# Performance work log

Measured on AMD Instinct MI355X. Metric: run time of the kernel, lower is better.

The kernel has to match this reference:

```python
import jax, jax.numpy as jnp
import numpy as np

B, C, H, W = 4, 512, 48, 48
BN_EPS = 1e-5


def setup_inputs() -> dict:
    key = jax.random.key(0)
    ks = jax.random.split(key, 12)
    s = 1.0 / np.sqrt(C)  # conv2d default init scale for 1x1 kernels
    return {
        "x": jax.random.normal(ks[0], (B, C, H, W), dtype=jnp.float32),
        "from_depth_estimation": jax.random.normal(ks[1], (B, C, H, W), dtype=jnp.float32),
        "w_rgb": jax.random.uniform(ks[2], (C, C), jnp.float32, -s, s),
        "b_rgb": jax.random.uniform(ks[3], (C,), jnp.float32, -s, s),
        "w_lhs": jax.random.uniform(ks[4], (C, C), jnp.float32, -s, s),
        "b_lhs": jax.random.uniform(ks[5], (C,), jnp.float32, -s, s),
        "w_rhs": jax.random.uniform(ks[6], (C, C), jnp.float32, -s, s),
        "b_rhs": jax.random.uniform(ks[7], (C,), jnp.float32, -s, s),
        "w_dec": jax.random.uniform(ks[8], (C, C), jnp.float32, -s, s),
        "b_dec": jax.random.uniform(ks[9], (C,), jnp.float32, -s, s),
        "gamma": jnp.ones((C,), jnp.float32),
        "beta": jnp.zeros((C,), jnp.float32),
    }


def _to_tokens(t):
    # (B,C,H,W) -> (B*H*W, C)
    return t.transpose(0, 2, 3, 1).reshape(-1, t.shape[1])


def reference(x, from_depth_estimation, w_rgb, b_rgb, w_lhs, b_lhs, w_rhs, b_rhs,
              w_dec, b_dec, gamma, beta):
    # 1x1 convs == per-token linear layers; weight layout (out, in)
    xt = _to_tokens(x) @ w_rgb.T + b_rgb          # (N, C)
    dt = _to_tokens(from_depth_estimation)
    lhs = dt @ w_lhs.T + b_lhs                     # (N, C)
    rhs = dt @ w_rhs.T + b_rhs                     # (N, C)

    # global, unscaled attention over all B*H*W tokens (batch dims mixed)
    logits = lhs @ rhs.T                           # (N, N)
    weight = jax.nn.softmax(logits, axis=1)
    enhanced = weight @ xt                         # (N, C)

    enhanced = enhanced.reshape(B, H, W, C).transpose(0, 3, 1, 2)  # (B,C,H,W)

    # decoder: 1x1 conv -> BatchNorm2d (batch stats, training mode) -> ReLU
    y = jnp.einsum('bchw,oc->bohw', enhanced, w_dec) + b_dec[None, :, None, None]
    mean = y.mean(axis=(0, 2, 3), keepdims=True)
    var = y.var(axis=(0, 2, 3), keepdims=True)     # biased variance (torch BN fwd)
    y = (y - mean) * jax.lax.rsqrt(var + BN_EPS)
    y = y * gamma[None, :, None, None] + beta[None, :, None, None]
    return jax.nn.relu(y)
```

## Files before the change

### kernel.cpp

```cpp
#include <hip/hip_runtime.h>
#include <math.h>

#define Bd 4
#define Cd 512
#define Hd 48
#define Wd 48
#define HWd (Hd * Wd)
#define Nd (Bd * HWd)
#define BN_EPS 1e-5f

#define QBLK 64
#define KBLK 128
#define NKS 4
#define KSLEN (Nd / NKS)
#define AITERS (KSLEN / KBLK)

typedef _Float16 half8 __attribute__((ext_vector_type(8)));
typedef _Float16 h4 __attribute__((ext_vector_type(4)));
typedef float f32x16 __attribute__((ext_vector_type(16)));

__device__ inline void gload_lds16(const void* g, void* l) {
    __builtin_amdgcn_global_load_lds((const __attribute__((address_space(1))) void*)g,
                                     (__attribute__((address_space(3))) void*)l, 16, 0, 0);
}

__device__ inline size_t wp_idx(int o, int c) {
    return (((size_t)(o >> 5) * 32 + (c >> 4)) * 64 + ((o & 31) + 32 * ((c >> 3) & 1))) * 8 + (c & 7);
}
__device__ inline size_t qp_idx(int q, int c) {
    return (((size_t)(q >> 5) * 64 + (c >> 3)) * 32 + (q & 31)) * 8 + (c & 7);
}
__device__ inline size_t kp_idx(int n, int o) {
    return ((((size_t)(n >> 7) * 4 + ((n >> 5) & 3)) * 32 + (o >> 4)) * 64
            + ((n & 31) + 32 * ((o >> 3) & 1))) * 8 + (o & 7);
}
__device__ inline size_t vp_idx(int n, int o) {
    return ((((size_t)(n >> 7) * 16 + (o >> 5)) * 8 + ((n >> 4) & 7)) * 64
            + ((o & 31) + 32 * ((n >> 3) & 1))) * 8 + (n & 7);
}

__global__ __launch_bounds__(256) void wpack_k(const float* __restrict__ w0,
                                               const float* __restrict__ w1,
                                               const float* __restrict__ w2,
                                               const float* __restrict__ w3,
                                               _Float16* __restrict__ p0,
                                               _Float16* __restrict__ p1,
                                               _Float16* __restrict__ p2,
                                               _Float16* __restrict__ p3) {
    const float* w; _Float16* p;
    switch (blockIdx.y) {
        case 0: w = w0; p = p0; break;
        case 1: w = w1; p = p1; break;
        case 2: w = w2; p = p2; break;
        default: w = w3; p = p3; break;
    }
    int idx = blockIdx.x * 256 + threadIdx.x;
    int o = idx >> 6;
    int cc = (idx & 63) * 8;
    float4 a = *(const float4*)(w + (size_t)o * 512 + cc);
    float4 b = *(const float4*)(w + (size_t)o * 512 + cc + 4);
    half8 v = {(_Float16)a.x, (_Float16)a.y, (_Float16)a.z, (_Float16)a.w,
               (_Float16)b.x, (_Float16)b.y, (_Float16)b.z, (_Float16)b.w};
    *(half8*)(p + wp_idx(o, cc)) = v;
}

template<int INM, int OUTM>
__global__ __launch_bounds__(256, 2) void linproj_k(const void* __restrict__ in,
                                                    const _Float16* __restrict__ Wp,
                                                    const float* __restrict__ bias,
                                                    void* __restrict__ outp) {
    constexpr bool SWAP = (OUTM == 2);
    __shared__ _Float16 Xs[16384];

    const int tid = threadIdx.x;
    const int wave = tid >> 6;
    const int lane = tid & 63;
    const int l31 = lane & 31;
    const int hi32 = lane >> 5;
    const int n0 = blockIdx.x * 32;
    const int by = blockIdx.y;
    const int b = n0 / HWd;
    const int hw0 = n0 % HWd;

    {
        const int t = tid & 31;
        const int c0 = tid >> 5;
        #pragma unroll 8
        for (int k = 0; k < 64; ++k) {
            int c = c0 + 8 * k;
            float val;
            if (INM == 0)
                val = ((const float*)in)[(size_t)(b * Cd + c) * HWd + hw0 + t];
            else
                val = (float)((const _Float16*)in)[(size_t)c * Nd + n0 + t];
            if (!SWAP)
                Xs[(c >> 3) * 256 + t * 8 + (c & 7)] = (_Float16)val;
            else
                Xs[(c >> 4) * 512 + (t + 32 * ((c >> 3) & 1)) * 8 + (c & 7)] = (_Float16)val;
        }
    }
    __syncthreads();

    #pragma unroll
    for (int ot = 0; ot < 2; ++ot) {
        const int otb = by * 256 + ot * 128 + wave * 32;

        half8 wa[32];
        const _Float16* wpb = Wp + ((size_t)(otb >> 5) * 32) * 512;
        #pragma unroll
        for (int f = 0; f < 32; ++f)
            wa[f] = *(const half8*)(wpb + (size_t)f * 512 + lane * 8);

        f32x16 acc;
        #pragma unroll
        for (int r = 0; r < 16; ++r) acc[r] = 0.f;

        __builtin_amdgcn_s_setprio(1);
        #pragma unroll
        for (int f = 0; f < 32; ++f) {
            if (!SWAP) {
                half8 xb = *(const half8*)(Xs + (2 * f + hi32) * 256 + l31 * 8);
                acc = __builtin_amdgcn_mfma_f32_32x32x16_f16(wa[f], xb, acc, 0, 0, 0);
            } else {
                half8 xa = *(const half8*)(Xs + f * 512 + lane * 8);
                acc = __builtin_amdgcn_mfma_f32_32x32x16_f16(xa, wa[f], acc, 0, 0, 0);
            }
        }
        __builtin_amdgcn_s_setprio(0);

        if (OUTM == 0) {
            _Float16* Qp = (_Float16*)outp;
            #pragma unroll
            for (int q8 = 0; q8 < 4; ++q8) {
                int o = otb + 8 * q8 + 4 * hi32;
                float4 bv = *(const float4*)(bias + o);
                h4 v = {(_Float16)(acc[4 * q8 + 0] + bv.x), (_Float16)(acc[4 * q8 + 1] + bv.y),
                        (_Float16)(acc[4 * q8 + 2] + bv.z), (_Float16)(acc[4 * q8 + 3] + bv.w)};
                *(h4*)(Qp + qp_idx(n0 + l31, o)) = v;
            }
        } else if (OUTM == 1) {
            _Float16* Kp = (_Float16*)outp;
            #pragma unroll
            for (int q8 = 0; q8 < 4; ++q8) {
                int o = otb + 8 * q8 + 4 * hi32;
                float4 bv = *(const float4*)(bias + o);
                h4 v = {(_Float16)(acc[4 * q8 + 0] + bv.x), (_Float16)(acc[4 * q8 + 1] + bv.y),
                        (_Float16)(acc[4 * q8 + 2] + bv.z), (_Float16)(acc[4 * q8 + 3] + bv.w)};
                *(h4*)(Kp + kp_idx(n0 + l31, o)) = v;
            }
        } else if (OUTM == 2) {
            _Float16* Vp = (_Float16*)outp;
            int o = otb + l31;
            float bc = bias[o];
            #pragma unroll
            for (int q8 = 0; q8 < 4; ++q8) {
                int n = n0 + 8 * q8 + 4 * hi32;
                h4 v = {(_Float16)(acc[4 * q8 + 0] + bc), (_Float16)(acc[4 * q8 + 1] + bc),
                        (_Float16)(acc[4 * q8 + 2] + bc), (_Float16)(acc[4 * q8 + 3] + bc)};
                *(h4*)(Vp + vp_idx(n, o)) = v;
            }
        } else {
            float* of = (float*)outp;
            #pragma unroll
            for (int r = 0; r < 16; ++r) {
                int o = otb + (r & 3) + 8 * (r >> 2) + 4 * hi32;
                of[(size_t)(b * Cd + o) * HWd + hw0 + l31] = acc[r] + bias[o];
            }
        }
    }
}

__global__ __launch_bounds__(512, 2) void attn_v10_k(
    const _Float16* __restrict__ Qp,
    const _Float16* __restrict__ Kp,
    const _Float16* __restrict__ Vp,
    _Float16* __restrict__ partH,
    float* __restrict__ marr,
    float* __restrict__ larr) {
    __shared__ _Float16 Qs[2 * 16384];
    __shared__ _Float16 Pl[8192];
    __shared__ float tm_s[4][64], ls_s[4][64];

    const int tid = threadIdx.x;
    const int wave = tid >> 6;
    const int lane = tid & 63;
    const int l31 = lane & 31;
    const int hi32 = lane >> 5;
    const int kt = wave & 3;
    const int qg = wave >> 2;
    const int ks = blockIdx.x & 3;
    const int qb = blockIdx.x >> 2;
    const int q0 = qb * QBLK;
    const int kbt0 = ks * AITERS;

    {
        const _Float16* Qt = Qp + (size_t)(q0 >> 5) * 16384;
        #pragma unroll
        for (int j = 0; j < 8; ++j)
            gload_lds16(Qt + (size_t)j * 4096 + tid * 8,
                        (char*)Qs + j * 8192 + wave * 1024);
    }
    __syncthreads();

    f32x16 o_acc[2][2];
    #pragma unroll
    for (int c = 0; c < 2; ++c)
        #pragma unroll
        for (int q = 0; q < 2; ++q)
            #pragma unroll
            for (int r = 0; r < 16; ++r) o_acc[c][q][r] = 0.f;
    float m0 = -INFINITY, m1 = -INFINITY, l0 = 0.f, l1 = 0.f;

    for (int it = 0; it < AITERS; ++it) {
        const _Float16* kp = Kp + ((size_t)(kbt0 + it) * 4 + kt) * 32 * 512;
        half8 ka[32];
        #pragma unroll
        for (int f = 0; f < 32; ++f)
            ka[f] = *(const half8*)(kp + (size_t)f * 512 + lane * 8);

        f32x16 s;
        #pragma unroll
        for (int r = 0; r < 16; ++r) s[r] = 0.f;
        const _Float16* qsb = Qs + qg * 16384;
        __builtin_amdgcn_s_setprio(1);
        #pragma unroll
        for (int f = 0; f < 32; ++f) {
            half8 qb8 = *(const half8*)(qsb + (2 * f + hi32) * 256 + l31 * 8);
            s = __builtin_amdgcn_mfma_f32_32x32x16_f16(ka[f], qb8, s, 0, 0, 0);
        }
        __builtin_amdgcn_s_setprio(0);

        float tmax = s[0];
        #pragma unroll
        for (int r = 1; r < 16; ++r) tmax = fmaxf(tmax, s[r]);
        tmax = fmaxf(tmax, __shfl_xor(tmax, 32));
        if (lane < 32) tm_s[kt][qg * 32 + lane] = tmax;
        __syncthreads();

        float mn0 = fmaxf(fmaxf(fmaxf(tm_s[0][l31], tm_s[1][l31]),
                                fmaxf(tm_s[2][l31], tm_s[3][l31])), m0);
        float mn1 = fmaxf(fmaxf(fmaxf(tm_s[0][32 + l31], tm_s[1][32 + l31]),
                                fmaxf(tm_s[2][32 + l31], tm_s[3][32 + l31])), m1);
        float corr0 = __expf(m0 - mn0);
        float corr1 = __expf(m1 - mn1);
        float mn_own = qg ? mn1 : mn0;

        float p[16];
        float psum = 0.f;
        #pragma unroll
        for (int r = 0; r < 16; ++r) { p[r] = __expf(s[r] - mn_own); psum += p[r]; }
        #pragma unroll
        for (int g = 0; g < 4; ++g) {
            h4 v = {(_Float16)p[4 * g + 0], (_Float16)p[4 * g + 1],
                    (_Float16)p[4 * g + 2], (_Float16)p[4 * g + 3]};
            *(h4*)(Pl + (qg * 8 + kt * 2 + (g >> 1)) * 512 + (g & 1) * 256
                      + l31 * 8 + 4 * hi32) = v;
        }
        psum += __shfl_xor(psum, 32);
        if (lane < 32) ls_s[kt][qg * 32 + lane] = psum;
        __syncthreads();

        l0 = l0 * corr0 + (ls_s[0][l31] + ls_s[1][l31]) + (ls_s[2][l31] + ls_s[3][l31]);
        l1 = l1 * corr1 + (ls_s[0][32 + l31] + ls_s[1][32 + l31])
                        + (ls_s[2][32 + l31] + ls_s[3][32 + l31]);
        m0 = mn0; m1 = mn1;

        half8 va[16];
        #pragma unroll
        for (int cht = 0; cht < 2; ++cht)
            #pragma unroll
            for (int kc = 0; kc < 8; ++kc)
                va[cht * 8 + kc] = *(const half8*)(
                    Vp + (((size_t)(kbt0 + it) * 16 + wave * 2 + cht) * 8 + kc) * 512
                       + lane * 8);

        #pragma unroll
        for (int cht = 0; cht < 2; ++cht)
            #pragma unroll
            for (int r = 0; r < 16; ++r) {
                o_acc[cht][0][r] *= corr0;
                o_acc[cht][1][r] *= corr1;
            }

        __builtin_amdgcn_s_setprio(1);
        #pragma unroll
        for (int qt = 0; qt < 2; ++qt)
            #pragma unroll
            for (int kc = 0; kc < 8; ++kc) {
                half8 pfrag = *(const half8*)(Pl + (qt * 8 + kc) * 512
                                                 + hi32 * 256 + l31 * 8);
                #pragma unroll
                for (int cht = 0; cht < 2; ++cht)
                    o_acc[cht][qt] = __builtin_amdgcn_mfma_f32_32x32x16_f16(
                        va[cht * 8 + kc], pfrag, o_acc[cht][qt], 0, 0, 0);
            }
        __builtin_amdgcn_s_setprio(0);
    }

    float li0 = 1.f / l0, li1 = 1.f / l1;
    #pragma unroll
    for (int cht = 0; cht < 2; ++cht)
        #pragma unroll
        for (int qt = 0; qt < 2; ++qt)
            #pragma unroll
            for (int r = 0; r < 16; ++r) {
                int row = (r & 3) + 8 * (r >> 2) + 4 * hi32;
                int ch = wave * 64 + cht * 32 + row;
                int q = q0 + qt * 32 + l31;
                __builtin_nontemporal_store(
                    (_Float16)(o_acc[cht][qt][r] * (qt ? li1 : li0)),
                    &partH[((size_t)ks * Cd + ch) * Nd + q]);
            }
    if (wave == 0 && lane < 32) {
        marr[(size_t)ks * Nd + q0 + lane] = m0;
        larr[(size_t)ks * Nd + q0 + lane] = l0;
        marr[(size_t)ks * Nd + q0 + 32 + lane] = m1;
        larr[(size_t)ks * Nd + q0 + 32 + lane] = l1;
    }
}

__global__ __launch_bounds__(256) void merge4_k(_Float16* __restrict__ partH,
                                                const float* __restrict__ marr,
                                                const float* __restrict__ larr) {
    size_t idx = (size_t)blockIdx.x * 256 + threadIdx.x;
    if (idx >= (size_t)Cd * Nd) return;
    int q = (int)(idx % Nd);
    float mv[NKS], wv[NKS];
    float mm = -INFINITY;
    #pragma unroll
    for (int s = 0; s < NKS; ++s) { mv[s] = marr[(size_t)s * Nd + q]; mm = fmaxf(mm, mv[s]); }
    float L = 0.f;
    #pragma unroll
    for (int s = 0; s < NKS; ++s) {
        wv[s] = larr[(size_t)s * Nd + q] * __expf(mv[s] - mm);
        L += wv[s];
    }
    float val = 0.f;
    #pragma unroll
    for (int s = 0; s < NKS; ++s)
        val += wv[s] * (float)partH[(size_t)s * Cd * Nd + idx];
    partH[idx] = (_Float16)(val / L);
}

__global__ __launch_bounds__(256) void bnstats_k(const float* __restrict__ y,
                                                 const float* __restrict__ gamma,
                                                 const float* __restrict__ beta,
                                                 float* __restrict__ stats) {
    const int c = blockIdx.x;
    const int tid = threadIdx.x;
    double s = 0.0, sq = 0.0;
    for (int b = 0; b < Bd; ++b) {
        const float* p = y + (size_t)(b * Cd + c) * HWd;
        for (int i = tid; i < HWd; i += 256) {
            double v = (double)p[i];
            s += v;
            sq += v * v;
        }
    }
    #pragma unroll
    for (int off = 32; off; off >>= 1) {
        s  += __shfl_xor(s, off, 64);
        sq += __shfl_xor(sq, off, 64);
    }
    __shared__ double ss[4], sqs[4];
    int wid = tid >> 6;
    if ((tid & 63) == 0) { ss[wid] = s; sqs[wid] = sq; }
    __syncthreads();
    if (tid == 0) {
        double S = ss[0] + ss[1] + ss[2] + ss[3];
        double Q = sqs[0] + sqs[1] + sqs[2] + sqs[3];
        double mean = S / (double)Nd;
        double var = Q / (double)Nd - mean * mean;
        float inv = (float)(1.0 / sqrt(var + (double)BN_EPS));
        float sc = gamma[c] * inv;
        stats[c] = sc;
        stats[Cd + c] = beta[c] - (float)mean * sc;
    }
}

__global__ __launch_bounds__(256) void bnapply_k(float* __restrict__ y,
                                                 const float* __restrict__ stats) {
    int idx = blockIdx.x * 256 + threadIdx.x;
    if (idx >= Bd * Cd * HWd) return;
    int c = (idx / HWd) % Cd;
    float v = fmaf(y[idx], stats[c], stats[Cd + c]);
    y[idx] = fmaxf(v, 0.f);
}

extern "C" void kernel_launch(void* const* d_in, const int* in_sizes, int n_in,
                              void* d_out, int out_size, void* d_ws, size_t ws_size,
                              hipStream_t stream) {
    const float* x     = (const float*)d_in[0];
    const float* depth = (const float*)d_in[1];
    const float* w_rgb = (const float*)d_in[2];
    const float* b_rgb = (const float*)d_in[3];
    const float* w_lhs = (const float*)d_in[4];
    const float* b_lhs = (const float*)d_in[5];
    const float* w_rhs = (const float*)d_in[6];
    const float* b_rhs = (const float*)d_in[7];
    const float* w_dec = (const float*)d_in[8];
    const float* b_dec = (const float*)d_in[9];
    const float* gamma = (const float*)d_in[10];
    const float* beta  = (const float*)d_in[11];
    float* out = (float*)d_out;

    char* wsb = (char*)d_ws;
    const size_t NC = (size_t)Nd * Cd;
    _Float16* Qp    = (_Float16*)wsb;
    _Float16* Kp    = (_Float16*)(wsb + NC * 2);
    _Float16* Vp    = (_Float16*)(wsb + NC * 4);
    _Float16* partH = (_Float16*)(wsb + NC * 6);
    float* marr  = (float*)(wsb + NC * 6 + (size_t)NKS * NC * 2);
    float* larr  = marr + (size_t)NKS * Nd;
    float* stats = larr + (size_t)NKS * Nd;
    _Float16* wpLhs = (_Float16*)(stats + 2 * Cd);
    _Float16* wpRhs = wpLhs + (size_t)Cd * Cd;
    _Float16* wpRgb = wpRhs + (size_t)Cd * Cd;
    _Float16* wpDec = wpRgb + (size_t)Cd * Cd;

    wpack_k<<<dim3(128, 4), 256, 0, stream>>>(w_lhs, w_rhs, w_rgb, w_dec,
                                              wpLhs, wpRhs, wpRgb, wpDec);

    dim3 gLin(Nd / 32, 2);
    linproj_k<0, 0><<<gLin, 256, 0, stream>>>(depth, wpLhs, b_lhs, Qp);
    linproj_k<0, 1><<<gLin, 256, 0, stream>>>(depth, wpRhs, b_rhs, Kp);
    linproj_k<0, 2><<<gLin, 256, 0, stream>>>(x, wpRgb, b_rgb, Vp);

    attn_v10_k<<<(Nd / QBLK) * NKS, 512, 0, stream>>>(Qp, Kp, Vp, partH, marr, larr);

    merge4_k<<<(int)((NC + 255) / 256), 256, 0, stream>>>(partH, marr, larr);

    linproj_k<3, 3><<<gLin, 256, 0, stream>>>(partH, wpDec, b_dec, out);

    bnstats_k<<<Cd, 256, 0, stream>>>(out, gamma, beta, stats);
    bnapply_k<<<(Bd * Cd * HWd + 255) / 256, 256, 0, stream>>>(out, stats);
}
```

Baseline: 379.2 us.

## Process two 128-key tiles per attention iteration to halve barriers

After: 425.1 us. 12.1% more time.

```diff
diff --git a/kernel.cpp b/kernel.cpp
--- a/kernel.cpp
+++ b/kernel.cpp
@@ -10,10 +10,11 @@
 #define BN_EPS 1e-5f
 
 #define QBLK 64
-#define KBLK 128
+#define KBLK 256
 #define NKS 4
 #define KSLEN (Nd / NKS)
 #define AITERS (KSLEN / KBLK)
+#define KT128 (KSLEN / 128)
 
 typedef _Float16 half8 __attribute__((ext_vector_type(8)));
 typedef _Float16 h4 __attribute__((ext_vector_type(4)));
@@ -170,7 +171,7 @@
     }
 }
 
-__global__ __launch_bounds__(512, 2) void attn_v10_k(
+__global__ __launch_bounds__(512, 2) void attn_v11_k(
     const _Float16* __restrict__ Qp,
     const _Float16* __restrict__ Kp,
     const _Float16* __restrict__ Vp,
@@ -178,8 +179,8 @@
     float* __restrict__ marr,
     float* __restrict__ larr) {
     __shared__ _Float16 Qs[2 * 16384];
-    __shared__ _Float16 Pl[8192];
-    __shared__ float tm_s[4][64], ls_s[4][64];
+    __shared__ _Float16 Pl[16384];
+    __shared__ float tm_s[8][64], ls_s[8][64];
 
     const int tid = threadIdx.x;
     const int wave = tid >> 6;
@@ -191,7 +192,7 @@
     const int ks = blockIdx.x & 3;
     const int qb = blockIdx.x >> 2;
     const int q0 = qb * QBLK;
-    const int kbt0 = ks * AITERS;
+    const int kbt0 = ks * KT128;
 
     {
         const _Float16* Qt = Qp + (size_t)(q0 >> 5) * 16384;
@@ -212,67 +213,93 @@
     float m0 = -INFINITY, m1 = -INFINITY, l0 = 0.f, l1 = 0.f;
 
     for (int it = 0; it < AITERS; ++it) {
-        const _Float16* kp = Kp + ((size_t)(kbt0 + it) * 4 + kt) * 32 * 512;
-        half8 ka[32];
-        #pragma unroll
-        for (int f = 0; f < 32; ++f)
-            ka[f] = *(const half8*)(kp + (size_t)f * 512 + lane * 8);
-
-        f32x16 s;
-        #pragma unroll
-        for (int r = 0; r < 16; ++r) s[r] = 0.f;
         const _Float16* qsb = Qs + qg * 16384;
-        __builtin_amdgcn_s_setprio(1);
-        #pragma unroll
-        for (int f = 0; f < 32; ++f) {
-            half8 qb8 = *(const half8*)(qsb + (2 * f + hi32) * 256 + l31 * 8);
-            s = __builtin_amdgcn_mfma_f32_32x32x16_f16(ka[f], qb8, s, 0, 0, 0);
-        }
-        __builtin_amdgcn_s_setprio(0);
-
-        float tmax = s[0];
-        #pragma unroll
-        for (int r = 1; r < 16; ++r) tmax = fmaxf(tmax, s[r]);
-        tmax = fmaxf(tmax, __shfl_xor(tmax, 32));
-        if (lane < 32) tm_s[kt][qg * 32 + lane] = tmax;
+
+        f32x16 s0, s1;
+        #pragma unroll
+        for (int r = 0; r < 16; ++r) { s0[r] = 0.f; s1[r] = 0.f; }
+        {
+            const _Float16* kp0 = Kp + ((size_t)((kbt0 + 2 * it) * 4 + kt)) * 32 * 512;
+            __builtin_amdgcn_s_setprio(1);
+            #pragma unroll
+            for (int f = 0; f < 32; ++f) {
+                half8 ka = *(const half8*)(kp0 + (size_t)f * 512 + lane * 8);
+                half8 qb8 = *(const half8*)(qsb + (2 * f + hi32) * 256 + l31 * 8);
+                s0 = __builtin_amdgcn_mfma_f32_32x32x16_f16(ka, qb8, s0, 0, 0, 0);
+            }
+            const _Float16* kp1 = Kp + ((size_t)((kbt0 + 2 * it + 1) * 4 + kt)) * 32 * 512;
+            #pragma unroll
+            for (int f = 0; f < 32; ++f) {
+                half8 ka = *(const half8*)(kp1 + (size_t)f * 512 + lane * 8);
+                half8 qb8 = *(const half8*)(qsb + (2 * f + hi32) * 256 + l31 * 8);
+                s1 = __builtin_amdgcn_mfma_f32_32x32x16_f16(ka, qb8, s1, 0, 0, 0);
+            }
+            __builtin_amdgcn_s_setprio(0);
+        }
+
+        float tmax0 = s0[0], tmax1 = s1[0];
+        #pragma unroll
+        for (int r = 1; r < 16; ++r) {
+            tmax0 = fmaxf(tmax0, s0[r]);
+            tmax1 = fmaxf(tmax1, s1[r]);
+        }
+        tmax0 = fmaxf(tmax0, __shfl_xor(tmax0, 32));
+        tmax1 = fmaxf(tmax1, __shfl_xor(tmax1, 32));
+        if (lane < 32) {
+            tm_s[kt][qg * 32 + lane] = tmax0;
+            tm_s[4 + kt][qg * 32 + lane] = tmax1;
+        }
         __syncthreads();
 
-        float mn0 = fmaxf(fmaxf(fmaxf(tm_s[0][l31], tm_s[1][l31]),
-                                fmaxf(tm_s[2][l31], tm_s[3][l31])), m0);
-        float mn1 = fmaxf(fmaxf(fmaxf(tm_s[0][32 + l31], tm_s[1][32 + l31]),
-                                fmaxf(tm_s[2][32 + l31], tm_s[3][32 + l31])), m1);
+        float mn0 = m0, mn1 = m1;
+        #pragma unroll
+        for (int t = 0; t < 8; ++t) {
+            mn0 = fmaxf(mn0, tm_s[t][l31]);
+            mn1 = fmaxf(mn1, tm_s[t][32 + l31]);
+        }
         float corr0 = __expf(m0 - mn0);
         float corr1 = __expf(m1 - mn1);
         float mn_own = qg ? mn1 : mn0;
 
-        float p[16];
-        float psum = 0.f;
-        #pragma unroll
-        for (int r = 0; r < 16; ++r) { p[r] = __expf(s[r] - mn_own); psum += p[r]; }
-        #pragma unroll
-        for (int g = 0; g < 4; ++g) {
-            h4 v = {(_Float16)p[4 * g + 0], (_Float16)p[4 * g + 1],
-                    (_Float16)p[4 * g + 2], (_Float16)p[4 * g + 3]};
-            *(h4*)(Pl + (qg * 8 + kt * 2 + (g >> 1)) * 512 + (g & 1) * 256
-                      + l31 * 8 + 4 * hi32) = v;
-        }
-        psum += __shfl_xor(psum, 32);
-        if (lane < 32) ls_s[kt][qg * 32 + lane] = psum;
+        float psum0 = 0.f, psum1 = 0.f;
+        {
+            float p[16];
+            #pragma unroll
+            for (int r = 0; r < 16; ++r) { p[r] = __expf(s0[r] - mn_own); psum0 += p[r]; }
+            #pragma unroll
+            for (int g = 0; g < 4; ++g) {
+                h4 v = {(_Float16)p[4 * g + 0], (_Float16)p[4 * g + 1],
+                        (_Float16)p[4 * g + 2], (_Float16)p[4 * g + 3]};
+                *(h4*)(Pl + (qg * 16 + kt * 2 + (g >> 1)) * 512 + (g & 1) * 256
+                          + l31 * 8 + 4 * hi32) = v;
+            }
+            #pragma unroll
+            for (int r = 0; r < 16; ++r) { p[r] = __expf(s1[r] - mn_own); psum1 += p[r]; }
+            #pragma unroll
+            for (int g = 0; g < 4; ++g) {
+                h4 v = {(_Float16)p[4 * g + 0], (_Float16)p[4 * g + 1],
+                        (_Float16)p[4 * g + 2], (_Float16)p[4 * g + 3]};
+                *(h4*)(Pl + (qg * 16 + 8 + kt * 2 + (g >> 1)) * 512 + (g & 1) * 256
+                          + l31 * 8 + 4 * hi32) = v;
+            }
+        }
+        psum0 += __shfl_xor(psum0, 32);
+        psum1 += __shfl_xor(psum1, 32);
+        if (lane < 32) {
+            ls_s[kt][qg * 32 + lane] = psum0;
+            ls_s[4 + kt][qg * 32 + lane] = psum1;
+        }
         __syncthreads();
 
-        l0 = l0 * corr0 + (ls_s[0][l31] + ls_s[1][l31]) + (ls_s[2][l31] + ls_s[3][l31]);
-        l1 = l1 * corr1 + (ls_s[0][32 + l31] + ls_s[1][32 + l31])
-                        + (ls_s[2][32 + l31] + ls_s[3][32 + l31]);
+        float add0 = 0.f, add1 = 0.f;
+        #pragma unroll
+        for (int t = 0; t < 8; ++t) {
+            add0 += ls_s[t][l31];
+            add1 += ls_s[t][32 + l31];
+        }
+        l0 = l0 * corr0 + add0;
+        l1 = l1 * corr1 + add1;
         m0 = mn0; m1 = mn1;
-
-        half8 va[16];
-        #pragma unroll
-        for (int cht = 0; cht < 2; ++cht)
-            #pragma unroll
-            for (int kc = 0; kc < 8; ++kc)
-                va[cht * 8 + kc] = *(const half8*)(
-                    Vp + (((size_t)(kbt0 + it) * 16 + wave * 2 + cht) * 8 + kc) * 512
-                       + lane * 8);
 
         #pragma unroll
         for (int cht = 0; cht < 2; ++cht)
@@ -282,19 +309,32 @@
                 o_acc[cht][1][r] *= corr1;
             }
 
-        __builtin_amdgcn_s_setprio(1);
-        #pragma unroll
-        for (int qt = 0; qt < 2; ++qt)
-            #pragma unroll
-            for (int kc = 0; kc < 8; ++kc) {
-                half8 pfrag = *(const half8*)(Pl + (qt * 8 + kc) * 512
-                                                 + hi32 * 256 + l31 * 8);
+        #pragma unroll
+        for (int h = 0; h < 2; ++h) {
+            const int kbt = kbt0 + 2 * it + h;
+            half8 va[16];
+            #pragma unroll
+            for (int cht = 0; cht < 2; ++cht)
                 #pragma unroll
-                for (int cht = 0; cht < 2; ++cht)
-                    o_acc[cht][qt] = __builtin_amdgcn_mfma_f32_32x32x16_f16(
-                        va[cht * 8 + kc], pfrag, o_acc[cht][qt], 0, 0, 0);
-            }
-        __builtin_amdgcn_s_setprio(0);
+                for (int kc = 0; kc < 8; ++kc)
+                    va[cht * 8 + kc] = *(const half8*)(
+                        Vp + (((size_t)kbt * 16 + wave * 2 + cht) * 8 + kc) * 512
+                           + lane * 8);
+
+            __builtin_amdgcn_s_setprio(1);
+            #pragma unroll
+            for (int qt = 0; qt < 2; ++qt)
+                #pragma unroll
+                for (int kc = 0; kc < 8; ++kc) {
+                    half8 pfrag = *(const half8*)(Pl + (qt * 16 + h * 8 + kc) * 512
+                                                     + hi32 * 256 + l31 * 8);
+                    #pragma unroll
+                    for (int cht = 0; cht < 2; ++cht)
+                        o_acc[cht][qt] = __builtin_amdgcn_mfma_f32_32x32x16_f16(
+                            va[cht * 8 + kc], pfrag, o_acc[cht][qt], 0, 0, 0);
+                }
+            __builtin_amdgcn_s_setprio(0);
+        }
     }
 
     float li0 = 1.f / l0, li1 = 1.f / l1;
@@ -426,7 +466,7 @@
     linproj_k<0, 1><<<gLin, 256, 0, stream>>>(depth, wpRhs, b_rhs, Kp);
     linproj_k<0, 2><<<gLin, 256, 0, stream>>>(x, wpRgb, b_rgb, Vp);
 
-    attn_v10_k<<<(Nd / QBLK) * NKS, 512, 0, stream>>>(Qp, Kp, Vp, partH, marr, larr);
+    attn_v11_k<<<(Nd / QBLK) * NKS, 512, 0, stream>>>(Qp, Kp, Vp, partH, marr, larr);
 
     merge4_k<<<(int)((NC + 255) / 256), 256, 0, stream>>>(partH, marr, larr);
 
```
